# Kernel optimization log

Hardware: AMD Instinct MI355X
Metric: run time of the kernel (lower is better)

Reference implementation:

```python
import jax
import jax.numpy as jnp
import numpy as np
from jax import lax

B, L, A, C = 32, 128, 64, 128  # batch, length, n_agents, channels (in == out)
KT = 3                          # temporal kernel size, padding (KT-1)//2 keeps length


def setup_inputs() -> dict:
    key = jax.random.key(0)
    k1, k2, k3 = jax.random.split(key, 3)
    x = jax.random.normal(k1, (B, L, A, C), dtype=jnp.float32)
    # Conv2d weight [out_ch, in_ch, kt, 1] and bias, kaiming-ish scale
    W = jax.random.normal(k2, (C, C, KT, 1), dtype=jnp.float32) * (1.0 / np.sqrt(C * KT))
    b = jax.random.normal(k3, (C,), dtype=jnp.float32) * 0.01
    return {"x": x, "W": W, "b": b}


def reference(x, W, b):
    # x: [B, L, A, C] -> [B, C, L, A] (torch NCHW layout with H=time, W=agents)
    length, n_agents = x.shape[1], x.shape[2]
    xc = jnp.transpose(x, (0, 3, 1, 2))
    res = xc  # residual is identity (input_dim == output_dim, t_stride == 1)
    pad_t = (KT - 1) // 2
    y = lax.conv_general_dilated(
        xc, W,
        window_strides=(1, 1),
        padding=[(pad_t, pad_t), (0, 0)],
        dimension_numbers=("NCHW", "OIHW", "NCHW"),
    ) + b[None, :, None, None]  # [B, C, L, A]
    # Dense graph g[t,a,t',a'] = 1 iff t==t' or a==a'.  einsum('ncv,vw->ncw', x, g)
    # is exactly: sum over same time (all agents) + sum over same agent (all times) - self.
    agent_sum = jnp.sum(y, axis=3, keepdims=True)  # [B, C, L, 1]
    time_sum = jnp.sum(y, axis=2, keepdims=True)   # [B, C, 1, A]
    scale = (length + n_agents - 2) ** 0.5
    g = (agent_sum + time_sum - y) / scale
    out = jax.nn.relu(g + res)
    return jnp.transpose(out, (0, 2, 3, 1))  # [B, L, A, C]
```

## Files before the change

### kernel.cpp

```cpp
#include <hip/hip_runtime.h>
#include <hip/hip_bf16.h>
#include <stdint.h>


typedef __attribute__((ext_vector_type(8))) short bf16x8;
typedef __attribute__((ext_vector_type(4))) float f32x4;

__device__ __forceinline__ uint32_t f2bf(float f) {
    union { __hip_bfloat16 b; uint16_t u; } cv;
    cv.b = __float2bfloat16(f);
    return (uint32_t)cv.u;
}
__device__ __forceinline__ float bf2f(uint32_t h) {
    union { uint32_t u; float f; } v; v.u = h << 16; return v.f;
}
__device__ __forceinline__ uint32_t pk2(float lo, float hi) {
    union { __hip_bfloat162 b; uint32_t u; } cv;
    cv.b = __float22bfloat162_rn(make_float2(lo, hi));
    return cv.u;
}

__global__ __launch_bounds__(256) void red_kernel(
    const float* __restrict__ x, float* __restrict__ xt_part,
    const float* __restrict__ W, uint16_t* __restrict__ wp)
{
    const int tid = threadIdx.x;
    const int bid = blockIdx.x;
    if (bid >= 512) {
        int o = (bid - 512) * 256 + tid;
        int i = o & 7, lane = (o >> 3) & 63, nt = (o >> 9) & 7, ks = (o >> 12) & 3, d = o >> 14;
        int ci = ks * 32 + (lane >> 4) * 8 + i;
        int co = nt * 16 + (lane & 15);
        wp[o] = (uint16_t)f2bf(W[(co * 128 + ci) * 3 + d]);
        return;
    }
    const int b = bid >> 4, g = bid & 15;
    const int ci8 = (tid & 15) * 8, ag = tid >> 4;

    float xtl[4][8];
    #pragma unroll
    for (int r = 0; r < 4; ++r)
        #pragma unroll
        for (int j = 0; j < 8; ++j) xtl[r][j] = 0.f;

    #pragma unroll
    for (int ti = 0; ti < 8; ++ti) {
        const int t = g * 8 + ti;
        const float* xr = x + ((size_t)(b * 128 + t) * 64) * 128;
        #pragma unroll
        for (int r = 0; r < 4; ++r) {
            const int a = ag * 4 + r;
            const float4 v0 = *(const float4*)(xr + a * 128 + ci8);
            const float4 v1 = *(const float4*)(xr + a * 128 + ci8 + 4);
            xtl[r][0] += v0.x; xtl[r][1] += v0.y; xtl[r][2] += v0.z; xtl[r][3] += v0.w;
            xtl[r][4] += v1.x; xtl[r][5] += v1.y; xtl[r][6] += v1.z; xtl[r][7] += v1.w;
        }
    }
    #pragma unroll
    for (int r = 0; r < 4; ++r) {
        float* p = xt_part + (((size_t)(b * 16 + g) * 64 + ag * 4 + r) * 128) + ci8;
        *(float4*)p       = make_float4(xtl[r][0], xtl[r][1], xtl[r][2], xtl[r][3]);
        *(float4*)(p + 4) = make_float4(xtl[r][4], xtl[r][5], xtl[r][6], xtl[r][7]);
    }
}

__global__ __launch_bounds__(256) void xtr_kernel(
    const float* __restrict__ xt_part, float* __restrict__ xt)
{
    const int idx = blockIdx.x * 256 + threadIdx.x;
    const int row = idx >> 4, ci8 = (idx & 15) * 8;
    const int b = row >> 6, a = row & 63;
    float s[8];
    #pragma unroll
    for (int j = 0; j < 8; ++j) s[j] = 0.f;
    #pragma unroll
    for (int g2 = 0; g2 < 16; ++g2) {
        const float* p = xt_part + (((size_t)(b * 16 + g2) * 64 + a) * 128) + ci8;
        const float4 v0 = *(const float4*)p;
        const float4 v1 = *(const float4*)(p + 4);
        s[0] += v0.x; s[1] += v0.y; s[2] += v0.z; s[3] += v0.w;
        s[4] += v1.x; s[5] += v1.y; s[6] += v1.z; s[7] += v1.w;
    }
    float* q = xt + (size_t)row * 128 + ci8;
    *(float4*)q       = make_float4(s[0], s[1], s[2], s[3]);
    *(float4*)(q + 4) = make_float4(s[4], s[5], s[6], s[7]);
}

__global__ __launch_bounds__(256, 2) void sums_kernel(
    const float* __restrict__ xt, const float* __restrict__ x,
    const uint16_t* __restrict__ wp, const float* __restrict__ bias,
    float* __restrict__ tsum)
{
    __shared__ __align__(16) uint16_t slab[128 * 128];
    const int tid = threadIdx.x;
    const int lane = tid & 63, wid = tid >> 6;
    const int wm = wid >> 1, wn = wid & 1;
    const int lr = lane & 15, lg = lane >> 4;
    f32x4 acc[4][4];
    #pragma unroll
    for (int mi = 0; mi < 4; ++mi)
        #pragma unroll
        for (int ni = 0; ni < 4; ++ni) acc[mi][ni] = (f32x4)0.f;

    const int bid = blockIdx.x;
    const int r = tid >> 1, h = tid & 1;
    const int grow = bid * 128 + r, sb = grow >> 6, sa = grow & 63;
    #pragma unroll
    for (int d = 0; d < 3; ++d) {
        {
            const float* Sp = xt + (size_t)grow * 128 + h * 64;
            const float* Ep = x + ((size_t)((sb * 128 + (d == 0 ? 127 : 0)) * 64 + sa)) * 128 + h * 64;
            #pragma unroll
            for (int k = 0; k < 8; ++k) {
                float4 f0 = *(const float4*)(Sp + k * 8);
                float4 f1 = *(const float4*)(Sp + k * 8 + 4);
                if (d != 1) {
                    const float4 e0 = *(const float4*)(Ep + k * 8);
                    const float4 e1 = *(const float4*)(Ep + k * 8 + 4);
                    f0.x -= e0.x; f0.y -= e0.y; f0.z -= e0.z; f0.w -= e0.w;
                    f1.x -= e1.x; f1.y -= e1.y; f1.z -= e1.z; f1.w -= e1.w;
                }
                uint4 o;
                o.x = pk2(f0.x, f0.y); o.y = pk2(f0.z, f0.w);
                o.z = pk2(f1.x, f1.y); o.w = pk2(f1.z, f1.w);
                const int sl = h * 8 + k;
                *(uint4*)(slab + r * 128 + (sl ^ (r & 7)) * 8) = o;
            }
        }
        __syncthreads();
        #pragma unroll
        for (int g = 0; g < 4; ++g) {
            bf16x8 bq[4], af[4];
            #pragma unroll
            for (int ni = 0; ni < 4; ++ni)
                bq[ni] = *(const bf16x8*)(wp + (size_t)((((d * 4 + g) * 8) + wn * 4 + ni) * 64 + lane) * 8);
            #pragma unroll
            for (int mi = 0; mi < 4; ++mi) {
                const int row = wm * 64 + mi * 16 + lr;
                af[mi] = *(const bf16x8*)(slab + row * 128 + ((g * 4 + lg) ^ (row & 7)) * 8);
            }
            #pragma unroll
            for (int mi = 0; mi < 4; ++mi)
                #pragma unroll
                for (int ni = 0; ni < 4; ++ni)
                    acc[mi][ni] = __builtin_amdgcn_mfma_f32_16x16x32_bf16(af[mi], bq[ni], acc[mi][ni], 0, 0, 0);
        }
        __syncthreads();
    }
    #pragma unroll
    for (int ni = 0; ni < 4; ++ni) {
        const int col = wn * 64 + ni * 16 + lr;
        const float bv = 128.f * bias[col];
        #pragma unroll
        for (int mi = 0; mi < 4; ++mi)
            #pragma unroll
            for (int j = 0; j < 4; ++j) {
                const int rg = bid * 128 + wm * 64 + mi * 16 + lg * 4 + j;
                tsum[(size_t)rg * 128 + col] = acc[mi][ni][j] + bv;
            }
    }
}

__global__ __launch_bounds__(512, 8) void conv_kernel(
    const float* __restrict__ x, const uint16_t* __restrict__ wp,
    const float* __restrict__ bias, const float* __restrict__ tsum,
    float* __restrict__ out)
{
    __shared__ __align__(16) uint16_t slab[192 * 64];
    __shared__ __align__(16) float asl[128];
    const int tid = threadIdx.x;
    const int raw = blockIdx.x;
    const int bid = (raw & 7) * 512 + (raw >> 3);
    const int b = bid >> 7, t = bid & 127;
    const int lane = tid & 63, wid = tid >> 6;
    const int lr = lane & 15, lg = lane >> 4;

    f32x4 acc[4];
    #pragma unroll
    for (int mi = 0; mi < 4; ++mi) acc[mi] = (f32x4)0.f;

#define STAGE(c) do {                                                          \
    _Pragma("unroll")                                                          \
    for (int k = 0; k < 3; ++k) {                                              \
        const int ro  = lane >> 3;                                             \
        const int row = wid * 24 + k * 8 + ro;                                 \
        const int gl  = (lane & 7) ^ ro;                                       \
        const int tloc = t + (row >> 6) - 1;                                   \
        uint4 o4 = make_uint4(0, 0, 0, 0);                                     \
        if ((unsigned)tloc < 128u) {                                           \
            const float* s_ = x +                                              \
                ((size_t)((b * 128 + tloc) * 64 + (row & 63))) * 128 +         \
                (c) * 64 + gl * 8;                                             \
            const float4 v0 = *(const float4*)s_;                              \
            const float4 v1 = *(const float4*)(s_ + 4);                        \
            o4.x = pk2(v0.x, v0.y); o4.y = pk2(v0.z, v0.w);                    \
            o4.z = pk2(v1.x, v1.y); o4.w = pk2(v1.z, v1.w);                    \
        }                                                                      \
        *(uint4*)(&slab[wid * 1536 + k * 512 + lane * 8]) = o4;                \
    } } while (0)

#define MFMA_CHUNK(c) do {                                                     \
    _Pragma("unroll")                                                          \
    for (int d = 0; d < 3; ++d)                                                \
        _Pragma("unroll")                                                      \
        for (int g2 = 0; g2 < 2; ++g2) {                                       \
            const int ks = (c) * 2 + g2;                                       \
            bf16x8 bq, af[4];                                                  \
            bq = *(const bf16x8*)(wp +                                         \
                (size_t)((((d * 4 + ks) * 8) + wid) * 64 + lane) * 8);         \
            _Pragma("unroll")                                                  \
            for (int mi = 0; mi < 4; ++mi) {                                   \
                const int row = d * 64 + mi * 16 + lr;                         \
                af[mi] = *(const bf16x8*)(&slab[row * 64 +                     \
                    (((g2 * 4 + lg) ^ (row & 7)) * 8)]);                       \
            }                                                                  \
            _Pragma("unroll")                                                  \
            for (int mi = 0; mi < 4; ++mi)                                     \
                acc[mi] = __builtin_amdgcn_mfma_f32_16x16x32_bf16(             \
                    af[mi], bq, acc[mi], 0, 0, 0);                             \
        } } while (0)

    STAGE(0);
    __syncthreads();
    MFMA_CHUNK(0);
    __syncthreads();
    STAGE(1);
    __syncthreads();
    MFMA_CHUNK(1);
    __syncthreads();

#undef STAGE
#undef MFMA_CHUNK

    {
        float p = 0.f;
        #pragma unroll
        for (int mi = 0; mi < 4; ++mi)
            #pragma unroll
            for (int j = 0; j < 4; ++j) p += acc[mi][j];
        p += __shfl_xor(p, 16);
        p += __shfl_xor(p, 32);
        const int col = wid * 16 + lr;
        if (lg == 0) asl[col] = p + 64.f * bias[col];
    }

    {
        const int col = wid * 16 + lr;
        const float bv = bias[col];
        const int cl = col & 63;
        const int rbase = (col >> 6) << 7;
        #pragma unroll
        for (int mi = 0; mi < 4; ++mi)
            #pragma unroll
            for (int j = 0; j < 4; ++j) {
                const int a = mi * 16 + lg * 4 + j;
                slab[(rbase + a) * 64 + (cl ^ ((a & 7) << 3))] = (uint16_t)f2bf(acc[mi][j] + bv);
            }
    }
    __syncthreads();

    {
        const float inv = 0.07254762501100116f;
        const int cg = tid & 15, rb = tid >> 4;
        const int cl8 = (cg & 7) * 8;
        const float4 as0 = *(const float4*)(asl + cg * 8);
        const float4 as1 = *(const float4*)(asl + cg * 8 + 4);
        const float av[8] = {as0.x, as0.y, as0.z, as0.w, as1.x, as1.y, as1.z, as1.w};
        #pragma unroll
        for (int j = 0; j < 2; ++j) {
            const int a = j * 32 + rb;
            const int swz = cl8 ^ ((a & 7) << 3);
            uint4 yv;
            float xx[8];
            if (cg < 8) {
                yv = *(const uint4*)(&slab[a * 64 + swz]);
                const float* xp = x + ((size_t)((b * 128 + t) * 64 + a)) * 128 + cg * 8;
                const float4 x0 = *(const float4*)xp, x1 = *(const float4*)(xp + 4);
                xx[0] = x0.x; xx[1] = x0.y; xx[2] = x0.z; xx[3] = x0.w;
                xx[4] = x1.x; xx[5] = x1.y; xx[6] = x1.z; xx[7] = x1.w;
            } else {
                yv = *(const uint4*)(&slab[(128 + a) * 64 + swz]);
                const uint4 xv = *(const uint4*)(&slab[(64 + a) * 64 + swz]);
                xx[0] = bf2f(xv.x & 0xFFFFu); xx[1] = bf2f(xv.x >> 16);
                xx[2] = bf2f(xv.y & 0xFFFFu); xx[3] = bf2f(xv.y >> 16);
                xx[4] = bf2f(xv.z & 0xFFFFu); xx[5] = bf2f(xv.z >> 16);
                xx[6] = bf2f(xv.w & 0xFFFFu); xx[7] = bf2f(xv.w >> 16);
            }
            const float* tp = tsum + ((size_t)(b * 64 + a)) * 128 + cg * 8;
            const float4 ts0 = *(const float4*)tp, ts1 = *(const float4*)(tp + 4);
            const float tv[8] = {ts0.x, ts0.y, ts0.z, ts0.w, ts1.x, ts1.y, ts1.z, ts1.w};
            float yy[8];
            yy[0] = bf2f(yv.x & 0xFFFFu); yy[1] = bf2f(yv.x >> 16);
            yy[2] = bf2f(yv.y & 0xFFFFu); yy[3] = bf2f(yv.y >> 16);
            yy[4] = bf2f(yv.z & 0xFFFFu); yy[5] = bf2f(yv.z >> 16);
            yy[6] = bf2f(yv.w & 0xFFFFu); yy[7] = bf2f(yv.w >> 16);
            float o[8];
            #pragma unroll
            for (int i = 0; i < 8; ++i) {
                const float gg = (av[i] + tv[i] - yy[i]) * inv + xx[i];
                o[i] = gg > 0.f ? gg : 0.f;
            }
            float* op = out + ((size_t)((b * 128 + t) * 64 + a)) * 128 + cg * 8;
            *(float4*)op       = make_float4(o[0], o[1], o[2], o[3]);
            *(float4*)(op + 4) = make_float4(o[4], o[5], o[6], o[7]);
        }
    }
}

extern "C" void kernel_launch(void* const* d_in, const int* in_sizes, int n_in,
                              void* d_out, int out_size, void* d_ws, size_t ws_size,
                              hipStream_t stream) {
    const float* x    = (const float*)d_in[0];
    const float* W    = (const float*)d_in[1];
    const float* bias = (const float*)d_in[2];
    float* out = (float*)d_out;

    char* ws = (char*)d_ws;
    uint16_t* wp    = (uint16_t*)(ws);
    float* xt_part  = (float*)(ws + 98304);
    float* xt       = (float*)(ws + 98304 + 16777216);
    float* tsum     = (float*)(ws + 98304 + 16777216 + 1048576);

    red_kernel  <<<704,  256, 0, stream>>>(x, xt_part, W, wp);
    xtr_kernel  <<<128,  256, 0, stream>>>(xt_part, xt);
    sums_kernel <<<16,   256, 0, stream>>>(xt, x, wp, bias, tsum);
    conv_kernel <<<4096, 512, 0, stream>>>(x, wp, bias, tsum, out);
}
```

Before: 116.0 us.

## Fuse partial-sum reduction into sums kernel and make conv blocks loop over tiles

```diff
diff --git a/kernel.cpp b/kernel.cpp
--- a/kernel.cpp
+++ b/kernel.cpp
@@ -64,33 +64,12 @@
     }
 }
 
-__global__ __launch_bounds__(256) void xtr_kernel(
-    const float* __restrict__ xt_part, float* __restrict__ xt)
-{
-    const int idx = blockIdx.x * 256 + threadIdx.x;
-    const int row = idx >> 4, ci8 = (idx & 15) * 8;
-    const int b = row >> 6, a = row & 63;
-    float s[8];
-    #pragma unroll
-    for (int j = 0; j < 8; ++j) s[j] = 0.f;
-    #pragma unroll
-    for (int g2 = 0; g2 < 16; ++g2) {
-        const float* p = xt_part + (((size_t)(b * 16 + g2) * 64 + a) * 128) + ci8;
-        const float4 v0 = *(const float4*)p;
-        const float4 v1 = *(const float4*)(p + 4);
-        s[0] += v0.x; s[1] += v0.y; s[2] += v0.z; s[3] += v0.w;
-        s[4] += v1.x; s[5] += v1.y; s[6] += v1.z; s[7] += v1.w;
-    }
-    float* q = xt + (size_t)row * 128 + ci8;
-    *(float4*)q       = make_float4(s[0], s[1], s[2], s[3]);
-    *(float4*)(q + 4) = make_float4(s[4], s[5], s[6], s[7]);
-}
-
 __global__ __launch_bounds__(256, 2) void sums_kernel(
-    const float* __restrict__ xt, const float* __restrict__ x,
+    const float* __restrict__ xt_part, const float* __restrict__ x,
     const uint16_t* __restrict__ wp, const float* __restrict__ bias,
     float* __restrict__ tsum)
 {
+    __shared__ float Sl[128 * 128];
     __shared__ __align__(16) uint16_t slab[128 * 128];
     const int tid = threadIdx.x;
     const int lane = tid & 63, wid = tid >> 6;
@@ -105,10 +84,35 @@
     const int bid = blockIdx.x;
     const int r = tid >> 1, h = tid & 1;
     const int grow = bid * 128 + r, sb = grow >> 6, sa = grow & 63;
+
+    {
+        const float* pb = xt_part + (((size_t)(sb * 16) * 64 + sa) * 128) + h * 64;
+        #pragma unroll
+        for (int c2 = 0; c2 < 4; ++c2) {
+            float s[16];
+            #pragma unroll
+            for (int j = 0; j < 16; ++j) s[j] = 0.f;
+            for (int g2 = 0; g2 < 16; ++g2) {
+                const float* p = pb + (size_t)g2 * 8192 + c2 * 16;
+                #pragma unroll
+                for (int q = 0; q < 4; ++q) {
+                    const float4 v = *(const float4*)(p + q * 4);
+                    s[q * 4 + 0] += v.x; s[q * 4 + 1] += v.y;
+                    s[q * 4 + 2] += v.z; s[q * 4 + 3] += v.w;
+                }
+            }
+            float* o = Sl + r * 128 + h * 64 + c2 * 16;
+            #pragma unroll
+            for (int q = 0; q < 4; ++q)
+                *(float4*)(o + q * 4) = make_float4(s[q*4], s[q*4+1], s[q*4+2], s[q*4+3]);
+        }
+    }
+    __syncthreads();
+
     #pragma unroll
     for (int d = 0; d < 3; ++d) {
         {
-            const float* Sp = xt + (size_t)grow * 128 + h * 64;
+            const float* Sp = Sl + r * 128 + h * 64;
             const float* Ep = x + ((size_t)((sb * 128 + (d == 0 ? 127 : 0)) * 64 + sa)) * 128 + h * 64;
             #pragma unroll
             for (int k = 0; k < 8; ++k) {
@@ -169,15 +173,10 @@
     __shared__ __align__(16) uint16_t slab[192 * 64];
     __shared__ __align__(16) float asl[128];
     const int tid = threadIdx.x;
-    const int raw = blockIdx.x;
-    const int bid = (raw & 7) * 512 + (raw >> 3);
-    const int b = bid >> 7, t = bid & 127;
+    const int p = blockIdx.x;
+    const int xcd = p & 7, q = p >> 3;
     const int lane = tid & 63, wid = tid >> 6;
     const int lr = lane & 15, lg = lane >> 4;
-
-    f32x4 acc[4];
-    #pragma unroll
-    for (int mi = 0; mi < 4; ++mi) acc[mi] = (f32x4)0.f;
 
 #define STAGE(c) do {                                                          \
     _Pragma("unroll")                                                          \
@@ -220,91 +219,101 @@
                     af[mi], bq, acc[mi], 0, 0, 0);                             \
         } } while (0)
 
-    STAGE(0);
-    __syncthreads();
-    MFMA_CHUNK(0);
-    __syncthreads();
-    STAGE(1);
-    __syncthreads();
-    MFMA_CHUNK(1);
-    __syncthreads();
+    for (int g = 0; g < 4; ++g) {
+        const int bid = xcd * 512 + g * 128 + q;
+        const int b = bid >> 7, t = bid & 127;
+
+        f32x4 acc[4];
+        #pragma unroll
+        for (int mi = 0; mi < 4; ++mi) acc[mi] = (f32x4)0.f;
+
+        STAGE(0);
+        __syncthreads();
+        MFMA_CHUNK(0);
+        __syncthreads();
+        STAGE(1);
+        __syncthreads();
+        MFMA_CHUNK(1);
+        __syncthreads();
+
+        {
+            float ps = 0.f;
+            #pragma unroll
+            for (int mi = 0; mi < 4; ++mi)
+                #pragma unroll
+                for (int j = 0; j < 4; ++j) ps += acc[mi][j];
+            ps += __shfl_xor(ps, 16);
+            ps += __shfl_xor(ps, 32);
+            const int col = wid * 16 + lr;
+            if (lg == 0) asl[col] = ps + 64.f * bias[col];
+        }
+
+        {
+            const int col = wid * 16 + lr;
+            const float bv = bias[col];
+            const int cl = col & 63;
+            const int rbase = (col >> 6) << 7;
+            #pragma unroll
+            for (int mi = 0; mi < 4; ++mi)
+                #pragma unroll
+                for (int j = 0; j < 4; ++j) {
+                    const int a = mi * 16 + lg * 4 + j;
+                    slab[(rbase + a) * 64 + (cl ^ ((a & 7) << 3))] = (uint16_t)f2bf(acc[mi][j] + bv);
+                }
+        }
+        __syncthreads();
+
+        {
+            const float inv = 0.07254762501100116f;
+            const int cg = tid & 15, rb = tid >> 4;
+            const int cl8 = (cg & 7) * 8;
+            const float4 as0 = *(const float4*)(asl + cg * 8);
+            const float4 as1 = *(const float4*)(asl + cg * 8 + 4);
+            const float av[8] = {as0.x, as0.y, as0.z, as0.w, as1.x, as1.y, as1.z, as1.w};
+            #pragma unroll
+            for (int j = 0; j < 2; ++j) {
+                const int a = j * 32 + rb;
+                const int swz = cl8 ^ ((a & 7) << 3);
+                uint4 yv;
+                float xx[8];
+                if (cg < 8) {
+                    yv = *(const uint4*)(&slab[a * 64 + swz]);
+                    const float* xp = x + ((size_t)((b * 128 + t) * 64 + a)) * 128 + cg * 8;
+                    const float4 x0 = *(const float4*)xp, x1 = *(const float4*)(xp + 4);
+                    xx[0] = x0.x; xx[1] = x0.y; xx[2] = x0.z; xx[3] = x0.w;
+                    xx[4] = x1.x; xx[5] = x1.y; xx[6] = x1.z; xx[7] = x1.w;
+                } else {
+                    yv = *(const uint4*)(&slab[(128 + a) * 64 + swz]);
+                    const uint4 xv = *(const uint4*)(&slab[(64 + a) * 64 + swz]);
+                    xx[0] = bf2f(xv.x & 0xFFFFu); xx[1] = bf2f(xv.x >> 16);
+                    xx[2] = bf2f(xv.y & 0xFFFFu); xx[3] = bf2f(xv.y >> 16);
+                    xx[4] = bf2f(xv.z & 0xFFFFu); xx[5] = bf2f(xv.z >> 16);
+                    xx[6] = bf2f(xv.w & 0xFFFFu); xx[7] = bf2f(xv.w >> 16);
+                }
+                const float* tp = tsum + ((size_t)(b * 64 + a)) * 128 + cg * 8;
+                const float4 ts0 = *(const float4*)tp, ts1 = *(const float4*)(tp + 4);
+                const float tv[8] = {ts0.x, ts0.y, ts0.z, ts0.w, ts1.x, ts1.y, ts1.z, ts1.w};
+                float yy[8];
+                yy[0] = bf2f(yv.x & 0xFFFFu); yy[1] = bf2f(yv.x >> 16);
+                yy[2] = bf2f(yv.y & 0xFFFFu); yy[3] = bf2f(yv.y >> 16);
+                yy[4] = bf2f(yv.z & 0xFFFFu); yy[5] = bf2f(yv.z >> 16);
+                yy[6] = bf2f(yv.w & 0xFFFFu); yy[7] = bf2f(yv.w >> 16);
+                float o[8];
+                #pragma unroll
+                for (int i = 0; i < 8; ++i) {
+                    const float gg = (av[i] + tv[i] - yy[i]) * inv + xx[i];
+                    o[i] = gg > 0.f ? gg : 0.f;
+                }
+                float* op = out + ((size_t)((b * 128 + t) * 64 + a)) * 128 + cg * 8;
+                *(float4*)op       = make_float4(o[0], o[1], o[2], o[3]);
+                *(float4*)(op + 4) = make_float4(o[4], o[5], o[6], o[7]);
+            }
+        }
+        __syncthreads();
+    }
 
 #undef STAGE
 #undef MFMA_CHUNK
-
-    {
-        float p = 0.f;
-        #pragma unroll
-        for (int mi = 0; mi < 4; ++mi)
-            #pragma unroll
-            for (int j = 0; j < 4; ++j) p += acc[mi][j];
-        p += __shfl_xor(p, 16);
-        p += __shfl_xor(p, 32);
-        const int col = wid * 16 + lr;
-        if (lg == 0) asl[col] = p + 64.f * bias[col];
-    }
-
-    {
-        const int col = wid * 16 + lr;
-        const float bv = bias[col];
-        const int cl = col & 63;
-        const int rbase = (col >> 6) << 7;
-        #pragma unroll
-        for (int mi = 0; mi < 4; ++mi)
-            #pragma unroll
-            for (int j = 0; j < 4; ++j) {
-                const int a = mi * 16 + lg * 4 + j;
-                slab[(rbase + a) * 64 + (cl ^ ((a & 7) << 3))] = (uint16_t)f2bf(acc[mi][j] + bv);
-            }
-    }
-    __syncthreads();
-
-    {
-        const float inv = 0.07254762501100116f;
-        const int cg = tid & 15, rb = tid >> 4;
-        const int cl8 = (cg & 7) * 8;
-        const float4 as0 = *(const float4*)(asl + cg * 8);
-        const float4 as1 = *(const float4*)(asl + cg * 8 + 4);
-        const float av[8] = {as0.x, as0.y, as0.z, as0.w, as1.x, as1.y, as1.z, as1.w};
-        #pragma unroll
-        for (int j = 0; j < 2; ++j) {
-            const int a = j * 32 + rb;
-            const int swz = cl8 ^ ((a & 7) << 3);
-            uint4 yv;
-            float xx[8];
-            if (cg < 8) {
-                yv = *(const uint4*)(&slab[a * 64 + swz]);
-                const float* xp = x + ((size_t)((b * 128 + t) * 64 + a)) * 128 + cg * 8;
-                const float4 x0 = *(const float4*)xp, x1 = *(const float4*)(xp + 4);
-                xx[0] = x0.x; xx[1] = x0.y; xx[2] = x0.z; xx[3] = x0.w;
-                xx[4] = x1.x; xx[5] = x1.y; xx[6] = x1.z; xx[7] = x1.w;
-            } else {
-                yv = *(const uint4*)(&slab[(128 + a) * 64 + swz]);
-                const uint4 xv = *(const uint4*)(&slab[(64 + a) * 64 + swz]);
-                xx[0] = bf2f(xv.x & 0xFFFFu); xx[1] = bf2f(xv.x >> 16);
-                xx[2] = bf2f(xv.y & 0xFFFFu); xx[3] = bf2f(xv.y >> 16);
-                xx[4] = bf2f(xv.z & 0xFFFFu); xx[5] = bf2f(xv.z >> 16);
-                xx[6] = bf2f(xv.w & 0xFFFFu); xx[7] = bf2f(xv.w >> 16);
-            }
-            const float* tp = tsum + ((size_t)(b * 64 + a)) * 128 + cg * 8;
-            const float4 ts0 = *(const float4*)tp, ts1 = *(const float4*)(tp + 4);
-            const float tv[8] = {ts0.x, ts0.y, ts0.z, ts0.w, ts1.x, ts1.y, ts1.z, ts1.w};
-            float yy[8];
-            yy[0] = bf2f(yv.x & 0xFFFFu); yy[1] = bf2f(yv.x >> 16);
-            yy[2] = bf2f(yv.y & 0xFFFFu); yy[3] = bf2f(yv.y >> 16);
-            yy[4] = bf2f(yv.z & 0xFFFFu); yy[5] = bf2f(yv.z >> 16);
-            yy[6] = bf2f(yv.w & 0xFFFFu); yy[7] = bf2f(yv.w >> 16);
-            float o[8];
-            #pragma unroll
-            for (int i = 0; i < 8; ++i) {
-                const float gg = (av[i] + tv[i] - yy[i]) * inv + xx[i];
-                o[i] = gg > 0.f ? gg : 0.f;
-            }
-            float* op = out + ((size_t)((b * 128 + t) * 64 + a)) * 128 + cg * 8;
-            *(float4*)op       = make_float4(o[0], o[1], o[2], o[3]);
-            *(float4*)(op + 4) = make_float4(o[4], o[5], o[6], o[7]);
-        }
-    }
 }
 
 extern "C" void kernel_launch(void* const* d_in, const int* in_sizes, int n_in,
@@ -318,11 +327,9 @@
     char* ws = (char*)d_ws;
     uint16_t* wp    = (uint16_t*)(ws);
     float* xt_part  = (float*)(ws + 98304);
-    float* xt       = (float*)(ws + 98304 + 16777216);
-    float* tsum     = (float*)(ws + 98304 + 16777216 + 1048576);
+    float* tsum     = (float*)(ws + 98304 + 16777216);
 
     red_kernel  <<<704,  256, 0, stream>>>(x, xt_part, W, wp);
-    xtr_kernel  <<<128,  256, 0, stream>>>(xt_part, xt);
-    sums_kernel <<<16,   256, 0, stream>>>(xt, x, wp, bias, tsum);
-    conv_kernel <<<4096, 512, 0, stream>>>(x, wp, bias, tsum, out);
-}
+    sums_kernel <<<16,   256, 0, stream>>>(xt_part, x, wp, bias, tsum);
+    conv_kernel <<<1024, 512, 0, stream>>>(x, wp, bias, tsum, out);
+}
```

New measurement: 256.7 us. 2.21x slower.
